# Performance work log

Hardware: AMD Instinct MI355X
Metric: run time of the kernel (lower is better)

The kernel has to match this reference:

```python
import jax, jax.numpy as jnp
import numpy as np

GROUP = 128  # per-group quantization along the input dimension


def _quantize_int4(w):
    """Asymmetric INT4 per-group quantization. w: [out, in] -> (q, scale, zero).
    q: int32 in [0,15], shape [out, in//GROUP, GROUP]; scale/zero: [out, in//GROUP]."""
    o, i = w.shape
    wg = w.reshape(o, i // GROUP, GROUP)
    mn = wg.min(axis=-1)
    mx = wg.max(axis=-1)
    scale = (mx - mn) / 15.0
    scale = jnp.where(scale == 0, jnp.float32(1.0), scale)
    zero = jnp.clip(jnp.round(-mn / scale), 0.0, 15.0)
    q = jnp.clip(jnp.round(wg / scale[..., None]) + zero[..., None], 0.0, 15.0).astype(jnp.int32)
    return q, scale.astype(jnp.float32), zero.astype(jnp.float32)


def _dequant(q, s, z):
    """(q - zero) * scale, regrouped back to [out, in]."""
    w = (q.astype(jnp.float32) - z[..., None]) * s[..., None]
    return w.reshape(q.shape[0], -1)


def setup_inputs() -> dict:
    key = jax.random.key(0)
    ks = jax.random.split(key, 5)
    B, D_IN, D_H, D_OUT = 512, 2048, 8192, 2048
    x = jax.random.normal(ks[0], (B, D_IN), dtype=jnp.float32)
    w1 = jax.random.normal(ks[1], (D_H, D_IN), dtype=jnp.float32) * 0.02
    b1 = jax.random.normal(ks[2], (D_H,), dtype=jnp.float32) * 0.01
    w2 = jax.random.normal(ks[3], (D_OUT, D_H), dtype=jnp.float32) * 0.02
    b2 = jax.random.normal(ks[4], (D_OUT,), dtype=jnp.float32) * 0.01
    q1, s1, z1 = _quantize_int4(w1)
    q2, s2, z2 = _quantize_int4(w2)
    return {"x": x, "q1": q1, "s1": s1, "z1": z1, "b1": b1,
            "q2": q2, "s2": s2, "z2": z2, "b2": b2}


def reference(x, q1, s1, z1, b1, q2, s2, z2, b2):
    # Layer 1: INT4 dequant + Linear + ReLU (fused in the native kernel)
    w1 = _dequant(q1, s1, z1)              # [D_H, D_IN]
    h = jax.nn.relu(x @ w1.T + b1)         # [B, D_H]
    # Layer 2: INT4 dequant + Linear (no activation)
    w2 = _dequant(q2, s2, z2)              # [D_OUT, D_H]
    return h @ w2.T + b2                   # [B, D_OUT]
```

## Files before the change

### kernel.cpp

```cpp
#include <hip/hip_runtime.h>
#include <stdint.h>

typedef unsigned short u16;
typedef __attribute__((ext_vector_type(8))) short bf16x8;
typedef __attribute__((ext_vector_type(8))) unsigned short u16x8;
typedef __attribute__((ext_vector_type(4))) float f32x4;
typedef __attribute__((ext_vector_type(4))) int i32x4;

__device__ __forceinline__ u16 f2bf(float f) {
  uint32_t u = __builtin_bit_cast(uint32_t, f);
  u += 0x7fffu + ((u >> 16) & 1u);
  return (u16)(u >> 16);
}

#define GLD16(g, l)                                                         \
  __builtin_amdgcn_global_load_lds(                                         \
      (const __attribute__((address_space(1))) void*)(g),                   \
      (__attribute__((address_space(3))) void*)(l), 16, 0, 0)


__global__ __launch_bounds__(256) void cvt_f32_bf16(const float* __restrict__ src,
                                                    u16* __restrict__ dst, int n8) {
  int t = blockIdx.x * 256 + threadIdx.x;
  if (t >= n8) return;
  f32x4 a = ((const f32x4*)src)[2 * t];
  f32x4 b = ((const f32x4*)src)[2 * t + 1];
  u16x8 o;
  o[0] = f2bf(a[0]); o[1] = f2bf(a[1]); o[2] = f2bf(a[2]); o[3] = f2bf(a[3]);
  o[4] = f2bf(b[0]); o[5] = f2bf(b[1]); o[6] = f2bf(b[2]); o[7] = f2bf(b[3]);
  ((u16x8*)dst)[t] = o;
}

__global__ __launch_bounds__(256) void dequant_w2x(const int* __restrict__ qa,
                                                   const float* __restrict__ sa,
                                                   const float* __restrict__ za,
                                                   u16* __restrict__ wa,
                                                   const int* __restrict__ qb,
                                                   const float* __restrict__ sb,
                                                   const float* __restrict__ zb,
                                                   u16* __restrict__ wb, int n8) {
  int t = blockIdx.x * 256 + threadIdx.x;
  if (t >= n8) return;
  const int* q = blockIdx.z ? qb : qa;
  const float* s = blockIdx.z ? sb : sa;
  const float* z = blockIdx.z ? zb : za;
  u16* w = blockIdx.z ? wb : wa;
  int g = t >> 4;
  float sc = s[g];
  float zp = z[g];
  i32x4 a = ((const i32x4*)q)[2 * t];
  i32x4 b = ((const i32x4*)q)[2 * t + 1];
  u16x8 o;
  o[0] = f2bf(((float)a[0] - zp) * sc);
  o[1] = f2bf(((float)a[1] - zp) * sc);
  o[2] = f2bf(((float)a[2] - zp) * sc);
  o[3] = f2bf(((float)a[3] - zp) * sc);
  o[4] = f2bf(((float)b[0] - zp) * sc);
  o[5] = f2bf(((float)b[1] - zp) * sc);
  o[6] = f2bf(((float)b[2] - zp) * sc);
  o[7] = f2bf(((float)b[3] - zp) * sc);
  ((u16x8*)w)[t] = o;
}

__global__ __launch_bounds__(256) void bias_init(float* __restrict__ out,
                                                 const float* __restrict__ b,
                                                 int N, int n4) {
  int t = blockIdx.x * 256 + threadIdx.x;
  if (t >= n4) return;
  int idx = t * 4;
  int n = idx & (N - 1);
  *(f32x4*)(out + idx) = *(const f32x4*)(b + n);
}

template <int NJ, bool RELU, bool OUT_BF16, bool ATOMIC>
__global__ __launch_bounds__(256) void gemm_bt(const u16* __restrict__ A,
                                               const u16* __restrict__ Bm,
                                               const float* __restrict__ bias,
                                               void* __restrict__ Cout,
                                               int N, int K, int kChunk) {
  __shared__ u16 As[2][128 * 32];
  __shared__ u16 Bs[2][32 * NJ * 32];
  const int tid = threadIdx.x;
  const int wave = tid >> 6;
  const int lane = tid & 63;
  const int m0 = blockIdx.y << 7;
  const int n0 = blockIdx.x * (32 * NJ);
  const int kStart = blockIdx.z * kChunk;
  const int srow = lane >> 2;
  const int scol = (((lane & 3) ^ ((lane >> 3) & 3)) << 3);
  const int wm = (wave >> 1) << 6;
  const int wn = (wave & 1) * (16 * NJ);
  const int quad = lane >> 4;
  const int l15 = lane & 15;
  const int cs = ((quad ^ ((l15 >> 1) & 3)) << 3);

  const u16* Ab = A + (size_t)(m0 + 32 * wave + srow) * K + kStart + scol;
  const u16* Bb = Bm + (size_t)(n0 + (8 * NJ) * wave + srow) * K + kStart + scol;
  const int ldsA = (32 * wave) * 32;
  const int ldsB = ((8 * NJ) * wave) * 32;
  const size_t rowskip = (size_t)16 * K;
  const int nT = kChunk >> 5;
  constexpr int VM = 2 + NJ / 2;

  f32x4 acc[4][NJ];
#pragma unroll
  for (int i = 0; i < 4; i++)
#pragma unroll
    for (int j = 0; j < NJ; j++) acc[i][j] = (f32x4){0.f, 0.f, 0.f, 0.f};

#define STAGE(bi_, t_)                                        \
  do {                                                        \
    const int ko_ = (t_) << 5;                                \
    GLD16(Ab + ko_, &As[bi_][ldsA]);                          \
    GLD16(Ab + ko_ + rowskip, &As[bi_][ldsA + 512]);          \
    GLD16(Bb + ko_, &Bs[bi_][ldsB]);                          \
    if (NJ == 4) GLD16(Bb + ko_ + rowskip, &Bs[bi_][ldsB + 512]); \
  } while (0)

  bf16x8 af[4], bf[NJ];
#define LOADFRAGS(bi_)                                                        \
  do {                                                                        \
    _Pragma("unroll") for (int i = 0; i < 4; i++)                             \
        af[i] = *(const bf16x8*)&As[bi_][(wm + i * 16 + l15) * 32 + cs];      \
    _Pragma("unroll") for (int j = 0; j < NJ; j++)                            \
        bf[j] = *(const bf16x8*)&Bs[bi_][(wn + j * 16 + l15) * 32 + cs];      \
  } while (0)

#define DOMFMA()                                                              \
  do {                                                                        \
    _Pragma("unroll") for (int i = 0; i < 4; i++)                             \
        _Pragma("unroll") for (int j = 0; j < NJ; j++)                        \
            acc[i][j] = __builtin_amdgcn_mfma_f32_16x16x32_bf16(              \
                af[i], bf[j], acc[i][j], 0, 0, 0);                            \
  } while (0)

  STAGE(0, 0);
  STAGE(1, 1);

  for (int t = 0; t < nT - 2; ++t) {
    asm volatile("s_waitcnt vmcnt(%0)" ::"i"(VM) : "memory");
    __builtin_amdgcn_s_barrier();
    LOADFRAGS(t & 1);
    asm volatile("s_waitcnt lgkmcnt(0)" ::: "memory");
    __builtin_amdgcn_sched_barrier(0);
    __builtin_amdgcn_s_barrier();
    STAGE(t & 1, t + 2);
    DOMFMA();
  }
  asm volatile("s_waitcnt vmcnt(%0)" ::"i"(VM) : "memory");
  __builtin_amdgcn_s_barrier();
  LOADFRAGS((nT - 2) & 1);
  asm volatile("s_waitcnt lgkmcnt(0)" ::: "memory");
  __builtin_amdgcn_sched_barrier(0);
  DOMFMA();
  asm volatile("s_waitcnt vmcnt(0)" ::: "memory");
  __builtin_amdgcn_s_barrier();
  LOADFRAGS((nT - 1) & 1);
  asm volatile("s_waitcnt lgkmcnt(0)" ::: "memory");
  __builtin_amdgcn_sched_barrier(0);
  DOMFMA();

#undef STAGE
#undef LOADFRAGS
#undef DOMFMA

#pragma unroll
  for (int i = 0; i < 4; i++) {
#pragma unroll
    for (int j = 0; j < NJ; j++) {
      const int col = n0 + wn + j * 16 + l15;
      float bv = 0.f;
      if (!ATOMIC) bv = bias[col];
#pragma unroll
      for (int r = 0; r < 4; r++) {
        const int row = m0 + wm + i * 16 + quad * 4 + r;
        float v = acc[i][j][r];
        if (ATOMIC) {
          atomicAdd((float*)Cout + (size_t)row * N + col, v);
        } else {
          v += bv;
          if (RELU) v = v > 0.f ? v : 0.f;
          if (OUT_BF16)
            ((u16*)Cout)[(size_t)row * N + col] = f2bf(v);
          else
            ((float*)Cout)[(size_t)row * N + col] = v;
        }
      }
    }
  }
}


extern "C" void kernel_launch(void* const* d_in, const int* in_sizes, int n_in,
                              void* d_out, int out_size, void* d_ws, size_t ws_size,
                              hipStream_t stream) {
  const float* x  = (const float*)d_in[0];
  const int*   q1 = (const int*)d_in[1];
  const float* s1 = (const float*)d_in[2];
  const float* z1 = (const float*)d_in[3];
  const float* b1 = (const float*)d_in[4];
  const int*   q2 = (const int*)d_in[5];
  const float* s2 = (const float*)d_in[6];
  const float* z2 = (const float*)d_in[7];
  const float* b2 = (const float*)d_in[8];
  float* out = (float*)d_out;

  const int B = 512, D_IN = 2048, D_H = 8192, D_OUT = 2048;

  char* ws = (char*)d_ws;
  u16* xb  = (u16*)(ws);
  u16* w1b = (u16*)(ws + (size_t)2 * 1024 * 1024);
  u16* hb  = (u16*)(ws + (size_t)34 * 1024 * 1024);
  u16* w2b = (u16*)(ws + (size_t)42 * 1024 * 1024);

  cvt_f32_bf16<<<(B * D_IN / 8 + 255) / 256, 256, 0, stream>>>(x, xb, B * D_IN / 8);
  {
    const int n8 = D_H * D_IN / 8;
    dim3 gd((n8 + 255) / 256, 1, 2);
    dequant_w2x<<<gd, 256, 0, stream>>>(q1, s1, z1, w1b, q2, s2, z2, w2b, n8);
  }
  {
    dim3 g1(D_H / 64, B / 128, 1);
    gemm_bt<2, true, true, false><<<g1, 256, 0, stream>>>(xb, w1b, b1, hb,
                                                          D_H, D_IN, D_IN);
  }
  bias_init<<<(B * D_OUT / 4 + 255) / 256, 256, 0, stream>>>(out, b2, D_OUT, B * D_OUT / 4);
  {
    dim3 g2(D_OUT / 128, B / 128, 16);
    gemm_bt<4, false, false, true><<<g2, 256, 0, stream>>>(hb, w2b, nullptr, out,
                                                           D_OUT, D_H, D_H / 16);
  }
}
```

Baseline: 269.5 us.

## Fuse INT4 dequantization into GEMM B-tile loading, drop separate dequant pass

Removes the standalone dequant kernel that wrote full bf16 copies of both weight matrices. Each GEMM now streams the int32 quantized weights straight into LDS, caches per-group scale and zero in shared memory, and converts to bf16 in registers with packed convert instructions before the MFMAs. This saves the write and re-read of about 64 MB of bf16 weights. The cost is twice as many bytes per B tile (int32 versus bf16), extra ALU work in the inner loop, and more LDS use. The second GEMM's split-K factor is also cut from 16 to 8.

```diff
diff --git a/kernel.cpp b/kernel.cpp
--- a/kernel.cpp
+++ b/kernel.cpp
@@ -2,10 +2,12 @@
 #include <stdint.h>
 
 typedef unsigned short u16;
+typedef unsigned int u32;
 typedef __attribute__((ext_vector_type(8))) short bf16x8;
 typedef __attribute__((ext_vector_type(8))) unsigned short u16x8;
 typedef __attribute__((ext_vector_type(4))) float f32x4;
 typedef __attribute__((ext_vector_type(4))) int i32x4;
+typedef __attribute__((ext_vector_type(4))) unsigned int u32x4;
 
 __device__ __forceinline__ u16 f2bf(float f) {
   uint32_t u = __builtin_bit_cast(uint32_t, f);
@@ -31,37 +33,6 @@
   ((u16x8*)dst)[t] = o;
 }
 
-__global__ __launch_bounds__(256) void dequant_w2x(const int* __restrict__ qa,
-                                                   const float* __restrict__ sa,
-                                                   const float* __restrict__ za,
-                                                   u16* __restrict__ wa,
-                                                   const int* __restrict__ qb,
-                                                   const float* __restrict__ sb,
-                                                   const float* __restrict__ zb,
-                                                   u16* __restrict__ wb, int n8) {
-  int t = blockIdx.x * 256 + threadIdx.x;
-  if (t >= n8) return;
-  const int* q = blockIdx.z ? qb : qa;
-  const float* s = blockIdx.z ? sb : sa;
-  const float* z = blockIdx.z ? zb : za;
-  u16* w = blockIdx.z ? wb : wa;
-  int g = t >> 4;
-  float sc = s[g];
-  float zp = z[g];
-  i32x4 a = ((const i32x4*)q)[2 * t];
-  i32x4 b = ((const i32x4*)q)[2 * t + 1];
-  u16x8 o;
-  o[0] = f2bf(((float)a[0] - zp) * sc);
-  o[1] = f2bf(((float)a[1] - zp) * sc);
-  o[2] = f2bf(((float)a[2] - zp) * sc);
-  o[3] = f2bf(((float)a[3] - zp) * sc);
-  o[4] = f2bf(((float)b[0] - zp) * sc);
-  o[5] = f2bf(((float)b[1] - zp) * sc);
-  o[6] = f2bf(((float)b[2] - zp) * sc);
-  o[7] = f2bf(((float)b[3] - zp) * sc);
-  ((u16x8*)w)[t] = o;
-}
-
 __global__ __launch_bounds__(256) void bias_init(float* __restrict__ out,
                                                  const float* __restrict__ b,
                                                  int N, int n4) {
@@ -72,35 +43,53 @@
   *(f32x4*)(out + idx) = *(const f32x4*)(b + n);
 }
 
-template <int NJ, bool RELU, bool OUT_BF16, bool ATOMIC>
-__global__ __launch_bounds__(256) void gemm_bt(const u16* __restrict__ A,
-                                               const u16* __restrict__ Bm,
-                                               const float* __restrict__ bias,
-                                               void* __restrict__ Cout,
-                                               int N, int K, int kChunk) {
+template <int NJ, int GC, bool RELU, bool OUT_BF16, bool ATOMIC>
+__global__ __launch_bounds__(256) void gemm_dqf(const u16* __restrict__ A,
+                                                const int* __restrict__ Q,
+                                                const float* __restrict__ S,
+                                                const float* __restrict__ Z,
+                                                const float* __restrict__ bias,
+                                                void* __restrict__ Cout,
+                                                int N, int K, int kChunk) {
+  constexpr int ROWS = 32 * NJ;
+  constexpr int SZST = 2 * GC + 2;
+  constexpr int VM = 2 + NJ;
   __shared__ u16 As[2][128 * 32];
-  __shared__ u16 Bs[2][32 * NJ * 32];
+  __shared__ int Bq[2][ROWS * 32];
+  __shared__ float szL[ROWS * SZST];
   const int tid = threadIdx.x;
   const int wave = tid >> 6;
   const int lane = tid & 63;
   const int m0 = blockIdx.y << 7;
-  const int n0 = blockIdx.x * (32 * NJ);
+  const int n0 = blockIdx.x * ROWS;
   const int kStart = blockIdx.z * kChunk;
   const int srow = lane >> 2;
-  const int scol = (((lane & 3) ^ ((lane >> 3) & 3)) << 3);
+  const int scolA = (((lane & 3) ^ ((lane >> 3) & 3)) << 3);
+  const int schB = (((lane & 7) ^ ((lane >> 3) & 7)) << 2);
   const int wm = (wave >> 1) << 6;
   const int wn = (wave & 1) * (16 * NJ);
   const int quad = lane >> 4;
   const int l15 = lane & 15;
-  const int cs = ((quad ^ ((l15 >> 1) & 3)) << 3);
-
-  const u16* Ab = A + (size_t)(m0 + 32 * wave + srow) * K + kStart + scol;
-  const u16* Bb = Bm + (size_t)(n0 + (8 * NJ) * wave + srow) * K + kStart + scol;
+  const int csA = ((quad ^ ((l15 >> 1) & 3)) << 3);
+
+  const u16* Ab = A + (size_t)(m0 + 32 * wave + srow) * K + kStart + scolA;
+  const int* Qb = Q + (size_t)(n0 + 8 * NJ * wave + (lane >> 3)) * K + kStart + schB;
   const int ldsA = (32 * wave) * 32;
-  const int ldsB = ((8 * NJ) * wave) * 32;
-  const size_t rowskip = (size_t)16 * K;
+  const int ldsB = (8 * NJ * wave) * 32;
+  const size_t rsA = (size_t)16 * K;
+  const size_t rsB = (size_t)8 * K;
   const int nT = kChunk >> 5;
-  constexpr int VM = 2 + NJ / 2;
+  const int nG = K >> 7;
+  const int g0 = kStart >> 7;
+
+  for (int p = tid; p < ROWS * GC; p += 256) {
+    const int r = p / GC;
+    const int gr = p - r * GC;
+    const size_t si = (size_t)(n0 + r) * nG + g0 + gr;
+    szL[r * SZST + 2 * gr] = S[si];
+    szL[r * SZST + 2 * gr + 1] = Z[si];
+  }
+  __syncthreads();
 
   f32x4 acc[4][NJ];
 #pragma unroll
@@ -108,22 +97,50 @@
 #pragma unroll
     for (int j = 0; j < NJ; j++) acc[i][j] = (f32x4){0.f, 0.f, 0.f, 0.f};
 
-#define STAGE(bi_, t_)                                        \
-  do {                                                        \
-    const int ko_ = (t_) << 5;                                \
-    GLD16(Ab + ko_, &As[bi_][ldsA]);                          \
-    GLD16(Ab + ko_ + rowskip, &As[bi_][ldsA + 512]);          \
-    GLD16(Bb + ko_, &Bs[bi_][ldsB]);                          \
-    if (NJ == 4) GLD16(Bb + ko_ + rowskip, &Bs[bi_][ldsB + 512]); \
+#define STAGE(bi_, t_)                                          \
+  do {                                                          \
+    const int ko_ = (t_) << 5;                                  \
+    GLD16(Ab + ko_, &As[bi_][ldsA]);                            \
+    GLD16(Ab + ko_ + rsA, &As[bi_][ldsA + 512]);                \
+    GLD16(Qb + ko_, &Bq[bi_][ldsB]);                            \
+    GLD16(Qb + ko_ + rsB, &Bq[bi_][ldsB + 256]);                \
+    if (NJ == 4) {                                              \
+      GLD16(Qb + ko_ + 2 * rsB, &Bq[bi_][ldsB + 512]);          \
+      GLD16(Qb + ko_ + 3 * rsB, &Bq[bi_][ldsB + 768]);          \
+    }                                                           \
   } while (0)
 
   bf16x8 af[4], bf[NJ];
-#define LOADFRAGS(bi_)                                                        \
+  i32x4 blo[NJ], bhi[NJ];
+  float2 bsz[NJ];
+#define LOADRAW(bi_, gRel_)                                                   \
   do {                                                                        \
     _Pragma("unroll") for (int i = 0; i < 4; i++)                             \
-        af[i] = *(const bf16x8*)&As[bi_][(wm + i * 16 + l15) * 32 + cs];      \
-    _Pragma("unroll") for (int j = 0; j < NJ; j++)                            \
-        bf[j] = *(const bf16x8*)&Bs[bi_][(wn + j * 16 + l15) * 32 + cs];      \
+        af[i] = *(const bf16x8*)&As[bi_][(wm + i * 16 + l15) * 32 + csA];     \
+    _Pragma("unroll") for (int j = 0; j < NJ; j++) {                          \
+      const int r_ = wn + j * 16 + l15;                                       \
+      const int s0_ = (((2 * quad) ^ (r_ & 7)) << 2);                         \
+      blo[j] = *(const i32x4*)&Bq[bi_][r_ * 32 + s0_];                        \
+      bhi[j] = *(const i32x4*)&Bq[bi_][r_ * 32 + (s0_ ^ 4)];                  \
+      bsz[j] = *(const float2*)&szL[r_ * SZST + 2 * (gRel_)];                 \
+    }                                                                         \
+  } while (0)
+
+#define CVTB()                                                                 \
+  do {                                                                         \
+    _Pragma("unroll") for (int j = 0; j < NJ; j++) {                           \
+      const float sc_ = bsz[j].x, zp_ = bsz[j].y;                              \
+      u32x4 w_;                                                                \
+      _Pragma("unroll") for (int c = 0; c < 2; c++) {                          \
+        float e0 = ((float)blo[j][2 * c] - zp_) * sc_;                         \
+        float e1 = ((float)blo[j][2 * c + 1] - zp_) * sc_;                     \
+        asm("v_cvt_pk_bf16_f32 %0, %1, %2" : "=v"(w_[c]) : "v"(e0), "v"(e1));  \
+        float e2 = ((float)bhi[j][2 * c] - zp_) * sc_;                         \
+        float e3 = ((float)bhi[j][2 * c + 1] - zp_) * sc_;                     \
+        asm("v_cvt_pk_bf16_f32 %0, %1, %2" : "=v"(w_[2 + c]) : "v"(e2), "v"(e3)); \
+      }                                                                        \
+      bf[j] = __builtin_bit_cast(bf16x8, w_);                                  \
+    }                                                                          \
   } while (0)
 
 #define DOMFMA()                                                              \
@@ -140,28 +157,32 @@
   for (int t = 0; t < nT - 2; ++t) {
     asm volatile("s_waitcnt vmcnt(%0)" ::"i"(VM) : "memory");
     __builtin_amdgcn_s_barrier();
-    LOADFRAGS(t & 1);
+    LOADRAW(t & 1, t >> 2);
     asm volatile("s_waitcnt lgkmcnt(0)" ::: "memory");
     __builtin_amdgcn_sched_barrier(0);
     __builtin_amdgcn_s_barrier();
     STAGE(t & 1, t + 2);
+    CVTB();
     DOMFMA();
   }
   asm volatile("s_waitcnt vmcnt(%0)" ::"i"(VM) : "memory");
   __builtin_amdgcn_s_barrier();
-  LOADFRAGS((nT - 2) & 1);
+  LOADRAW((nT - 2) & 1, (nT - 2) >> 2);
   asm volatile("s_waitcnt lgkmcnt(0)" ::: "memory");
   __builtin_amdgcn_sched_barrier(0);
+  CVTB();
   DOMFMA();
   asm volatile("s_waitcnt vmcnt(0)" ::: "memory");
   __builtin_amdgcn_s_barrier();
-  LOADFRAGS((nT - 1) & 1);
+  LOADRAW((nT - 1) & 1, (nT - 1) >> 2);
   asm volatile("s_waitcnt lgkmcnt(0)" ::: "memory");
   __builtin_amdgcn_sched_barrier(0);
+  CVTB();
   DOMFMA();
 
 #undef STAGE
-#undef LOADFRAGS
+#undef LOADRAW
+#undef CVTB
 #undef DOMFMA
 
 #pragma unroll
@@ -208,26 +229,19 @@
   const int B = 512, D_IN = 2048, D_H = 8192, D_OUT = 2048;
 
   char* ws = (char*)d_ws;
-  u16* xb  = (u16*)(ws);
-  u16* w1b = (u16*)(ws + (size_t)2 * 1024 * 1024);
-  u16* hb  = (u16*)(ws + (size_t)34 * 1024 * 1024);
-  u16* w2b = (u16*)(ws + (size_t)42 * 1024 * 1024);
+  u16* xb = (u16*)(ws);
+  u16* hb = (u16*)(ws + (size_t)2 * 1024 * 1024);
 
   cvt_f32_bf16<<<(B * D_IN / 8 + 255) / 256, 256, 0, stream>>>(x, xb, B * D_IN / 8);
   {
-    const int n8 = D_H * D_IN / 8;
-    dim3 gd((n8 + 255) / 256, 1, 2);
-    dequant_w2x<<<gd, 256, 0, stream>>>(q1, s1, z1, w1b, q2, s2, z2, w2b, n8);
-  }
-  {
     dim3 g1(D_H / 64, B / 128, 1);
-    gemm_bt<2, true, true, false><<<g1, 256, 0, stream>>>(xb, w1b, b1, hb,
-                                                          D_H, D_IN, D_IN);
+    gemm_dqf<2, 16, true, true, false><<<g1, 256, 0, stream>>>(
+        xb, q1, s1, z1, b1, hb, D_H, D_IN, D_IN);
   }
   bias_init<<<(B * D_OUT / 4 + 255) / 256, 256, 0, stream>>>(out, b2, D_OUT, B * D_OUT / 4);
   {
-    dim3 g2(D_OUT / 128, B / 128, 16);
-    gemm_bt<4, false, false, true><<<g2, 256, 0, stream>>>(hb, w2b, nullptr, out,
-                                                           D_OUT, D_H, D_H / 16);
-  }
-}
+    dim3 g2(D_OUT / 128, B / 128, 8);
+    gemm_dqf<4, 8, false, false, true><<<g2, 256, 0, stream>>>(
+        hb, q2, s2, z2, nullptr, out, D_OUT, D_H, D_H / 8);
+  }
+}
```

New measurement: 273.1 us. Within noise of the previous version (+1.4%).

## Use 256x256 split-K MFMA GEMM for layer one with separate ReLU conversion

Applied to the files above, without the earlier changes.

Layer one now runs on a new 512-thread kernel with 256x256 tiles, a 64-wide K step, double-buffered direct-to-LDS loads and explicit wait and priority scheduling. K is split four ways with fp32 atomics into a bias-initialised buffer, and a separate kernel then applies ReLU and converts to bf16. The split-K factor for layer two is halved. Larger tiles raise operand reuse and MFMA density, and split-K fills the GPU, in exchange for extra atomics, an fp32 intermediate round-trip and two more launches.

```diff
diff --git a/kernel.cpp b/kernel.cpp
--- a/kernel.cpp
+++ b/kernel.cpp
@@ -72,6 +72,160 @@
   *(f32x4*)(out + idx) = *(const f32x4*)(b + n);
 }
 
+__global__ __launch_bounds__(256) void relu_cvt(const float* __restrict__ h32,
+                                                u16* __restrict__ hb, int n8) {
+  int t = blockIdx.x * 256 + threadIdx.x;
+  if (t >= n8) return;
+  f32x4 a = ((const f32x4*)h32)[2 * t];
+  f32x4 b = ((const f32x4*)h32)[2 * t + 1];
+  u16x8 o;
+#pragma unroll
+  for (int e = 0; e < 4; e++) {
+    float va = a[e] > 0.f ? a[e] : 0.f;
+    float vb = b[e] > 0.f ? b[e] : 0.f;
+    o[e] = f2bf(va);
+    o[e + 4] = f2bf(vb);
+  }
+  ((u16x8*)hb)[t] = o;
+}
+
+__global__ __launch_bounds__(512, 2) void gemm256d(const u16* __restrict__ A,
+                                                   const u16* __restrict__ Bm,
+                                                   float* __restrict__ Cout,
+                                                   int N, int K, int kChunk) {
+  __shared__ u16 As[2][256 * 64];
+  __shared__ u16 Bs[2][256 * 64];
+  const int tid = threadIdx.x;
+  const int wave = tid >> 6;
+  const int lane = tid & 63;
+  const int m0 = blockIdx.y << 8;
+  const int n0 = blockIdx.x << 8;
+  const int kStart = blockIdx.z * kChunk;
+  const int srow = lane >> 3;
+  const int schunk = (((lane & 7) ^ (srow & 7)) << 3);
+  const int wm = (wave >> 2) << 7;
+  const int wn = (wave & 3) << 6;
+  const int quad = lane >> 4;
+  const int l15 = lane & 15;
+  const int x7 = lane & 7;
+  const int c0 = ((quad ^ x7) << 3);
+  const int c1 = (((4 | quad) ^ x7) << 3);
+
+  const u16* Ab = A + (size_t)(m0 + 32 * wave + srow) * K + kStart + schunk;
+  const u16* Bb = Bm + (size_t)(n0 + 32 * wave + srow) * K + kStart + schunk;
+  const int ldsW = (32 * wave) * 64;
+  const size_t rs8 = (size_t)8 * K;
+  const int nT = kChunk >> 6;
+
+  f32x4 acc[8][4];
+#pragma unroll
+  for (int i = 0; i < 8; i++)
+#pragma unroll
+    for (int j = 0; j < 4; j++) acc[i][j] = (f32x4){0.f, 0.f, 0.f, 0.f};
+
+#define STAGE(bi_, t_)                                          \
+  do {                                                          \
+    const int ko_ = (t_) << 6;                                  \
+    GLD16(Ab + ko_,           &As[bi_][ldsW]);                  \
+    GLD16(Ab + ko_ + rs8,     &As[bi_][ldsW + 512]);            \
+    GLD16(Ab + ko_ + 2 * rs8, &As[bi_][ldsW + 1024]);           \
+    GLD16(Ab + ko_ + 3 * rs8, &As[bi_][ldsW + 1536]);           \
+    GLD16(Bb + ko_,           &Bs[bi_][ldsW]);                  \
+    GLD16(Bb + ko_ + rs8,     &Bs[bi_][ldsW + 512]);            \
+    GLD16(Bb + ko_ + 2 * rs8, &Bs[bi_][ldsW + 1024]);           \
+    GLD16(Bb + ko_ + 3 * rs8, &Bs[bi_][ldsW + 1536]);           \
+  } while (0)
+
+  bf16x8 af0[8], bf0[4], af1[8], bf1[4];
+#define LOADFRAGS(bi_)                                                          \
+  do {                                                                          \
+    _Pragma("unroll") for (int i = 0; i < 8; i++)                               \
+        af0[i] = *(const bf16x8*)&As[bi_][(wm + i * 16 + l15) * 64 + c0];       \
+    _Pragma("unroll") for (int j = 0; j < 4; j++)                               \
+        bf0[j] = *(const bf16x8*)&Bs[bi_][(wn + j * 16 + l15) * 64 + c0];       \
+    _Pragma("unroll") for (int i = 0; i < 8; i++)                               \
+        af1[i] = *(const bf16x8*)&As[bi_][(wm + i * 16 + l15) * 64 + c1];       \
+    _Pragma("unroll") for (int j = 0; j < 4; j++)                               \
+        bf1[j] = *(const bf16x8*)&Bs[bi_][(wn + j * 16 + l15) * 64 + c1];       \
+  } while (0)
+
+#define MFMA_S0()                                                               \
+  do {                                                                          \
+    __builtin_amdgcn_s_setprio(1);                                              \
+    _Pragma("unroll") for (int i = 0; i < 8; i++)                               \
+        _Pragma("unroll") for (int j = 0; j < 4; j++)                           \
+            acc[i][j] = __builtin_amdgcn_mfma_f32_16x16x32_bf16(                \
+                af0[i], bf0[j], acc[i][j], 0, 0, 0);                            \
+    __builtin_amdgcn_s_setprio(0);                                              \
+  } while (0)
+
+#define MFMA_S1()                                                               \
+  do {                                                                          \
+    __builtin_amdgcn_s_setprio(1);                                              \
+    _Pragma("unroll") for (int i = 0; i < 8; i++)                               \
+        _Pragma("unroll") for (int j = 0; j < 4; j++)                           \
+            acc[i][j] = __builtin_amdgcn_mfma_f32_16x16x32_bf16(                \
+                af1[i], bf1[j], acc[i][j], 0, 0, 0);                            \
+    __builtin_amdgcn_s_setprio(0);                                              \
+  } while (0)
+
+  STAGE(0, 0);
+  STAGE(1, 1);
+
+  int bi = 0;
+  for (int t = 0; t < nT - 2; ++t) {
+    asm volatile("s_waitcnt vmcnt(8)" ::: "memory");
+    __builtin_amdgcn_s_barrier();
+    LOADFRAGS(bi);
+    asm volatile("s_waitcnt lgkmcnt(12)" ::: "memory");
+    __builtin_amdgcn_sched_barrier(0);
+    MFMA_S0();
+    asm volatile("s_waitcnt lgkmcnt(0)" ::: "memory");
+    __builtin_amdgcn_sched_barrier(0);
+    __builtin_amdgcn_s_barrier();
+    STAGE(bi, t + 2);
+    MFMA_S1();
+    bi ^= 1;
+  }
+  asm volatile("s_waitcnt vmcnt(8)" ::: "memory");
+  __builtin_amdgcn_s_barrier();
+  LOADFRAGS(bi);
+  asm volatile("s_waitcnt lgkmcnt(12)" ::: "memory");
+  __builtin_amdgcn_sched_barrier(0);
+  MFMA_S0();
+  asm volatile("s_waitcnt lgkmcnt(0)" ::: "memory");
+  __builtin_amdgcn_sched_barrier(0);
+  MFMA_S1();
+  bi ^= 1;
+  asm volatile("s_waitcnt vmcnt(0)" ::: "memory");
+  __builtin_amdgcn_s_barrier();
+  LOADFRAGS(bi);
+  asm volatile("s_waitcnt lgkmcnt(12)" ::: "memory");
+  __builtin_amdgcn_sched_barrier(0);
+  MFMA_S0();
+  asm volatile("s_waitcnt lgkmcnt(0)" ::: "memory");
+  __builtin_amdgcn_sched_barrier(0);
+  MFMA_S1();
+
+#undef STAGE
+#undef LOADFRAGS
+#undef MFMA_S0
+#undef MFMA_S1
+
+#pragma unroll
+  for (int i = 0; i < 8; i++) {
+#pragma unroll
+    for (int j = 0; j < 4; j++) {
+      const int col = n0 + wn + j * 16 + l15;
+#pragma unroll
+      for (int r = 0; r < 4; r++) {
+        const int row = m0 + wm + i * 16 + quad * 4 + r;
+        atomicAdd(Cout + (size_t)row * N + col, acc[i][j][r]);
+      }
+    }
+  }
+}
+
 template <int NJ, bool RELU, bool OUT_BF16, bool ATOMIC>
 __global__ __launch_bounds__(256) void gemm_bt(const u16* __restrict__ A,
                                                const u16* __restrict__ Bm,
@@ -208,10 +362,11 @@
   const int B = 512, D_IN = 2048, D_H = 8192, D_OUT = 2048;
 
   char* ws = (char*)d_ws;
-  u16* xb  = (u16*)(ws);
-  u16* w1b = (u16*)(ws + (size_t)2 * 1024 * 1024);
-  u16* hb  = (u16*)(ws + (size_t)34 * 1024 * 1024);
-  u16* w2b = (u16*)(ws + (size_t)42 * 1024 * 1024);
+  u16*   xb  = (u16*)(ws);
+  u16*   w1b = (u16*)(ws + (size_t)2 * 1024 * 1024);
+  u16*   hb  = (u16*)(ws + (size_t)34 * 1024 * 1024);
+  u16*   w2b = (u16*)(ws + (size_t)42 * 1024 * 1024);
+  float* h32 = (float*)(ws + (size_t)74 * 1024 * 1024);
 
   cvt_f32_bf16<<<(B * D_IN / 8 + 255) / 256, 256, 0, stream>>>(x, xb, B * D_IN / 8);
   {
@@ -219,15 +374,16 @@
     dim3 gd((n8 + 255) / 256, 1, 2);
     dequant_w2x<<<gd, 256, 0, stream>>>(q1, s1, z1, w1b, q2, s2, z2, w2b, n8);
   }
+  bias_init<<<(B * D_H / 4 + 255) / 256, 256, 0, stream>>>(h32, b1, D_H, B * D_H / 4);
   {
-    dim3 g1(D_H / 64, B / 128, 1);
-    gemm_bt<2, true, true, false><<<g1, 256, 0, stream>>>(xb, w1b, b1, hb,
-                                                          D_H, D_IN, D_IN);
-  }
+    dim3 g1(D_H / 256, B / 256, 4);
+    gemm256d<<<g1, 512, 0, stream>>>(xb, w1b, h32, D_H, D_IN, D_IN / 4);
+  }
+  relu_cvt<<<(B * D_H / 8 + 255) / 256, 256, 0, stream>>>(h32, hb, B * D_H / 8);
   bias_init<<<(B * D_OUT / 4 + 255) / 256, 256, 0, stream>>>(out, b2, D_OUT, B * D_OUT / 4);
   {
-    dim3 g2(D_OUT / 128, B / 128, 16);
+    dim3 g2(D_OUT / 128, B / 128, 8);
     gemm_bt<4, false, false, true><<<g2, 256, 0, stream>>>(hb, w2b, nullptr, out,
-                                                           D_OUT, D_H, D_H / 16);
-  }
-}
+                                                           D_OUT, D_H, D_H / 8);
+  }
+}
```

Result: slower. 293.5 us (+8.9%).
